# Kernel tuning notes

Measured on AMD Instinct MI355X. Metric: run time of the kernel, lower is better.

The kernel has to match this reference:

```python
import jax, jax.numpy as jnp
import numpy as np

DIL = 2      # dilation of deformable depthwise conv (padding == dilation -> same size)
EPS = 1e-5   # BatchNorm eps
B, C, O, G, H, W = 4, 256, 256, 64, 64, 64


def conv2d(x, w, padding, dilation=1):
    return jax.lax.conv_general_dilated(
        x, w, window_strides=(1, 1), padding=[(padding, padding)] * 2,
        rhs_dilation=(dilation, dilation),
        dimension_numbers=("NCHW", "OIHW", "NCHW"))


def bn_inf(x, gamma, beta, mean, var):
    scale = (gamma / jnp.sqrt(var + EPS))[None, :, None, None]
    return (x - mean[None, :, None, None]) * scale + beta[None, :, None, None]


def bilinear_gather(xt, ys, xs):
    # xt: [B,H,W,C]; ys, xs: [B,K,H,W] float sample coords. Zero padding outside.
    Bb, Hh, Ww, Cc = xt.shape
    y0 = jnp.floor(ys)
    x0 = jnp.floor(xs)
    wy = (ys - y0)[..., None]
    wx = (xs - x0)[..., None]
    bidx = jnp.arange(Bb)[:, None, None, None]

    def gather(yi, xi):
        valid = (yi >= 0) & (yi < Hh) & (xi >= 0) & (xi < Ww)
        yc = jnp.clip(yi, 0, Hh - 1).astype(jnp.int32)
        xc = jnp.clip(xi, 0, Ww - 1).astype(jnp.int32)
        val = xt[bidx, yc, xc]            # [B,K,H,W,C]
        return val * valid[..., None].astype(xt.dtype)

    v00 = gather(y0, x0)
    v01 = gather(y0, x0 + 1)
    v10 = gather(y0 + 1, x0)
    v11 = gather(y0 + 1, x0 + 1)
    return (v00 * (1 - wy) * (1 - wx) + v01 * (1 - wy) * wx
            + v10 * wy * (1 - wx) + v11 * wy * wx)


def setup_inputs() -> dict:
    key = jax.random.key(0)
    ks = jax.random.split(key, 12)
    inp = {
        "x": jax.random.normal(ks[0], (B, C, H, W), jnp.float32),
        "grad_feats": jax.random.normal(ks[1], (B, G, H, W), jnp.float32),
        # offset block: conv3x3(G->18) + BN + ReLU
        "off_w": jax.random.normal(ks[2], (18, G, 3, 3), jnp.float32) / np.sqrt(G * 9),
        "off_gamma": 1.0 + 0.1 * jax.random.normal(ks[3], (18,), jnp.float32),
        "off_beta": 0.1 * jax.random.normal(ks[4], (18,), jnp.float32),
        "off_mean": 0.1 * jax.random.normal(ks[5], (18,), jnp.float32),
        "off_var": jax.random.uniform(ks[6], (18,), jnp.float32, 0.5, 1.5),
        # deformable separable conv: depthwise 3x3 (per-channel) then pointwise 1x1, no bias
        "dw_w": jax.random.normal(ks[7], (C, 3, 3), jnp.float32) / 3.0,
        "pw_w": jax.random.normal(ks[8], (O, C), jnp.float32) / np.sqrt(C),
        # output BN
        "bn_gamma": 1.0 + 0.1 * jax.random.normal(ks[9], (O,), jnp.float32),
        "bn_beta": 0.1 * jax.random.normal(ks[10], (O,), jnp.float32),
        "bn_mean": 0.1 * jax.random.normal(ks[11], (O,), jnp.float32),
        "bn_var": jnp.ones((O,), jnp.float32),
    }
    return inp


def reference(x, grad_feats, off_w, off_gamma, off_beta, off_mean, off_var,
              dw_w, pw_w, bn_gamma, bn_beta, bn_mean, bn_var):
    Bb, Cc, Hh, Ww = x.shape
    # offset block: conv3x3 + BN + ReLU -> [B,18,H,W]
    off = jax.nn.relu(bn_inf(conv2d(grad_feats, off_w, 1),
                             off_gamma, off_beta, off_mean, off_var))
    off = off.reshape(Bb, 9, 2, Hh, Ww)
    dy, dx = off[:, :, 0], off[:, :, 1]                     # [B,9,H,W]
    # base kernel grid: padding == dilation so tap offsets are (kh-1)*DIL
    kk = (jnp.arange(3, dtype=jnp.float32) - 1.0) * DIL
    ky = jnp.repeat(kk, 3)                                   # [9] row offsets
    kx = jnp.tile(kk, 3)                                     # [9] col offsets
    gy = jnp.arange(Hh, dtype=jnp.float32)[None, None, :, None] + ky[None, :, None, None] + dy
    gx = jnp.arange(Ww, dtype=jnp.float32)[None, None, None, :] + kx[None, :, None, None] + dx
    samp = bilinear_gather(x.transpose(0, 2, 3, 1), gy, gx)  # [B,9,H,W,C]
    out = jnp.einsum("bkhwc,ck->bchw", samp, dw_w.reshape(Cc, 9))   # depthwise
    out = jnp.einsum("bchw,oc->bohw", out, pw_w)                    # pointwise 1x1
    out = jax.nn.relu(bn_inf(out, bn_gamma, bn_beta, bn_mean, bn_var))
    return out
```

## Files before the change

kernel.cpp:

```cpp
#include <hip/hip_runtime.h>
#include <stdint.h>

#define Bn 4
#define Cn 256
#define On 256
#define Gn 64
#define Hn 64
#define Wn 64
#define HWn 4096
#define EPSf 1e-5f

#define WS_XT    0u
#define WS_OFF   8388608u
#define WS_PWB   9568256u
#define WS_WT    9699328u

typedef __attribute__((ext_vector_type(8))) short short8;
typedef __attribute__((ext_vector_type(4))) float f4;

__device__ __forceinline__ unsigned int bfround(float f) {
    unsigned int u = __float_as_uint(f);
    u += 0x7FFFu + ((u >> 16) & 1u);
    return u >> 16;
}
__device__ __forceinline__ float blo(unsigned u) { return __uint_as_float(u << 16); }
__device__ __forceinline__ float bhi(unsigned u) { return __uint_as_float(u & 0xFFFF0000u); }

__global__ __launch_bounds__(256, 4) void k_pre(const float* __restrict__ x,
                                                const float* __restrict__ pw_w,
                                                const float* __restrict__ off_w,
                                                char* __restrict__ ws)
{
    __shared__ float smem[4160];
    int tid = threadIdx.x, bid = blockIdx.x;

    if (bid < 1024) {
        unsigned short* xt = (unsigned short*)(ws + WS_XT);
        int pt = bid & 63, ct = (bid >> 6) & 3, b = bid >> 8;
        int p0 = pt * 64, c0 = ct * 64;
        const f4* x4 = (const f4*)(x + (size_t)b * Cn * HWn);
        #pragma unroll
        for (int it = 0; it < 4; ++it) {
            int v = it * 256 + tid;
            int ci = v >> 4, pj = v & 15;
            f4 f = __builtin_nontemporal_load(&x4[(size_t)(c0 + ci) * 1024 + (p0 >> 2) + pj]);
            smem[ci * 65 + pj * 4 + 0] = f[0];
            smem[ci * 65 + pj * 4 + 1] = f[1];
            smem[ci * 65 + pj * 4 + 2] = f[2];
            smem[ci * 65 + pj * 4 + 3] = f[3];
        }
        __syncthreads();
        unsigned short* xtb = xt + (size_t)b * HWn * Cn;
        #pragma unroll
        for (int it = 0; it < 2; ++it) {
            int u = it * 256 + tid;
            int pi = u >> 3, cj = u & 7;
            float f[8];
            #pragma unroll
            for (int j = 0; j < 8; ++j)
                f[j] = smem[(cj * 8 + j) * 65 + pi];
            uint4 pk;
            pk.x = bfround(f[0]) | (bfround(f[1]) << 16);
            pk.y = bfround(f[2]) | (bfround(f[3]) << 16);
            pk.z = bfround(f[4]) | (bfround(f[5]) << 16);
            pk.w = bfround(f[6]) | (bfround(f[7]) << 16);
            *(uint4*)(xtb + (size_t)(p0 + pi) * Cn + c0 + cj * 8) = pk;
        }
        return;
    }
    if (bid < 1056) {
        unsigned short* pwb = (unsigned short*)(ws + WS_PWB);
        const float4* p4 = (const float4*)pw_w;
        uint2* o2 = (uint2*)pwb;
        int base = (bid - 1024) * 512;
        #pragma unroll
        for (int i = 0; i < 2; ++i) {
            int id2 = base + i * 256 + tid;
            float4 f = p4[id2];
            uint2 pk;
            pk.x = bfround(f.x) | (bfround(f.y) << 16);
            pk.y = bfround(f.z) | (bfround(f.w) << 16);
            o2[id2] = pk;
        }
        return;
    }
    {
        float* wT = (float*)(ws + WS_WT);
        for (int i = tid; i < 10368; i += 256) {
            int ch = i / 576;
            int rem = i - ch * 576;
            int g = rem / 9;
            int r9 = rem - g * 9;
            int ty = r9 / 3, tx = r9 - ty * 3;
            wT[(g * 3 + ty) * 54 + tx * 18 + ch] = off_w[i];
        }
    }
}

__global__ __launch_bounds__(256, 4) void k_off(const float* __restrict__ gf,
                                                const float* __restrict__ og,
                                                const float* __restrict__ obt,
                                                const float* __restrict__ om,
                                                const float* __restrict__ ov,
                                                char* __restrict__ ws)
{
    __shared__ float swt[10368];
    __shared__ float sred[4 * 18 * 65];
    const float* __restrict__ wT = (const float*)(ws + WS_WT);
    float* __restrict__ off = (float*)(ws + WS_OFF);
    int tid = threadIdx.x;
    int h = blockIdx.x, b = blockIdx.y;
    int lane = tid & 63;
    int wvU = __builtin_amdgcn_readfirstlane(tid >> 6);

    {
        const float4* w4 = (const float4*)wT;
        float4* s4 = (float4*)swt;
        #pragma unroll
        for (int j = 0; j < 11; ++j) {
            int idx = j * 256 + tid;
            if (idx < 2592) s4[idx] = w4[idx];
        }
    }
    __syncthreads();

    float acc[18];
    #pragma unroll
    for (int ch = 0; ch < 18; ++ch) acc[ch] = 0.f;

    const float* gfb = gf + (size_t)b * Gn * HWn;
    #pragma unroll 2
    for (int gi = 0; gi < 16; ++gi) {
        int g = wvU * 16 + gi;
        const float* gfg = gfb + (size_t)g * HWn;
        float rv[3], su[3], sd[3];
        #pragma unroll
        for (int r = 0; r < 3; ++r) {
            int y = h - 1 + r;
            rv[r] = ((unsigned)y < 64u) ? gfg[y * 64 + lane] : 0.f;
        }
        #pragma unroll
        for (int r = 0; r < 3; ++r) {
            float u = __shfl_up(rv[r], 1);   su[r] = (lane == 0)  ? 0.f : u;
            float d = __shfl_down(rv[r], 1); sd[r] = (lane == 63) ? 0.f : d;
        }
        #pragma unroll
        for (int ty = 0; ty < 3; ++ty) {
            const float* wrow = &swt[(g * 3 + ty) * 54];
            #pragma unroll
            for (int ch = 0; ch < 18; ++ch)
                acc[ch] += wrow[ch] * su[ty] + wrow[18 + ch] * rv[ty] + wrow[36 + ch] * sd[ty];
        }
    }

    #pragma unroll
    for (int ch = 0; ch < 18; ++ch)
        sred[(wvU * 18 + ch) * 65 + lane] = acc[ch];
    __syncthreads();

    float* obp = off + (size_t)(b * HWn + h * 64) * 18;
    for (int i = tid; i < 1152; i += 256) {
        int w = i / 18, ch = i - w * 18;
        float v = sred[ch * 65 + w] + sred[(18 + ch) * 65 + w]
                + sred[(36 + ch) * 65 + w] + sred[(54 + ch) * 65 + w];
        float s = og[ch] * rsqrtf(ov[ch] + EPSf);
        v = (v - om[ch]) * s + obt[ch];
        obp[i] = v > 0.f ? v : 0.f;
    }
}

#define TLD 264
__global__ __launch_bounds__(512, 4) void k_fuse(float* __restrict__ out,
                                                 const float* __restrict__ dw_w,
                                                 const float* __restrict__ bg,
                                                 const float* __restrict__ bb,
                                                 const float* __restrict__ bm,
                                                 const float* __restrict__ bv,
                                                 const char* __restrict__ ws)
{
    const unsigned short* __restrict__ xt  = (const unsigned short*)(ws + WS_XT);
    const unsigned short* __restrict__ pwb = (const unsigned short*)(ws + WS_PWB);
    const float* __restrict__ off = (const float*)(ws + WS_OFF);
    __shared__ float smeta[288 * 8];
    __shared__ float sdw[9 * 256];
    __shared__ unsigned short tl[32 * TLD];

    int bid = blockIdx.x;
    int xcd = bid & 7, slot = bid >> 3;
    int b = xcd >> 1;
    int h = ((xcd & 1) << 5) | (slot >> 1);
    int w0 = (slot & 1) << 5;
    int tid = threadIdx.x;

    for (int i = tid; i < 2304; i += 512) {
        int k = i >> 8, c = i & 255;
        sdw[i] = dw_w[c * 9 + k];
    }

    if (tid < 288) {
        int k = tid >> 5, wl = tid & 31;
        int w = w0 + wl;
        int kyi = k / 3, kxi = k - kyi * 3;
        const float* op = off + ((size_t)(b * HWn + h * 64 + w)) * 18 + 2 * k;
        float dy = op[0], dx = op[1];
        float gy = (float)(h + (kyi - 1) * 2) + dy;
        float gx = (float)(w + (kxi - 1) * 2) + dx;
        float fy = floorf(gy), fx = floorf(gx);
        float wy = gy - fy, wx = gx - fx;
        int y0 = (int)fy, x0 = (int)fx;
        int y1 = y0 + 1, x1 = x0 + 1;
        float m00 = ((unsigned)y0 < 64u && (unsigned)x0 < 64u) ? 1.f : 0.f;
        float m01 = ((unsigned)y0 < 64u && (unsigned)x1 < 64u) ? 1.f : 0.f;
        float m10 = ((unsigned)y1 < 64u && (unsigned)x0 < 64u) ? 1.f : 0.f;
        float m11 = ((unsigned)y1 < 64u && (unsigned)x1 < 64u) ? 1.f : 0.f;
        int y0c = min(max(y0, 0), 63), y1c = min(max(y1, 0), 63);
        int x0c = min(max(x0, 0), 63), x1c = min(max(x1, 0), 63);
        float4 mw;
        mw.x = (1.f - wy) * (1.f - wx) * m00;
        mw.y = (1.f - wy) * wx * m01;
        mw.z = wy * (1.f - wx) * m10;
        mw.w = wy * wx * m11;
        float4 mo;
        mo.x = __int_as_float((y0c * 64 + x0c) << 9);
        mo.y = __int_as_float((y0c * 64 + x1c) << 9);
        mo.z = __int_as_float((y1c * 64 + x0c) << 9);
        mo.w = __int_as_float((y1c * 64 + x1c) << 9);
        float4* s4w = (float4*)smeta;
        s4w[(k * 32 + wl) * 2] = mw;
        s4w[(k * 32 + wl) * 2 + 1] = mo;
    }
    __syncthreads();

    int lane = tid & 63, wave = tid >> 6;
    int half = lane >> 5, c8 = lane & 31;
    int c0 = c8 * 8;

    const char* xb = (const char*)(xt + (size_t)b * HWn * Cn);
    int laneByte = c8 * 16;
    const float4* s4 = (const float4*)smeta;
    #pragma unroll
    for (int iter = 0; iter < 2; ++iter) {
        int wl = iter * 16 + wave * 2 + half;
        float acc[8];
        #pragma unroll
        for (int j = 0; j < 8; ++j) acc[j] = 0.f;
        #pragma unroll 1
        for (int k = 0; k < 9; ++k) {
            float4 mw = s4[(k * 32 + wl) * 2];
            float4 mo = s4[(k * 32 + wl) * 2 + 1];
            float4 d0 = *(const float4*)(&sdw[k * 256 + c0]);
            float4 d1 = *(const float4*)(&sdw[k * 256 + c0 + 4]);
            uint4 qA = *(const uint4*)(xb + __float_as_int(mo.x) + laneByte);
            uint4 qB = *(const uint4*)(xb + __float_as_int(mo.y) + laneByte);
            uint4 qC = *(const uint4*)(xb + __float_as_int(mo.z) + laneByte);
            uint4 qD = *(const uint4*)(xb + __float_as_int(mo.w) + laneByte);
            const unsigned* uA = (const unsigned*)&qA;
            const unsigned* uB = (const unsigned*)&qB;
            const unsigned* uC = (const unsigned*)&qC;
            const unsigned* uD = (const unsigned*)&qD;
            const float* dk0 = (const float*)&d0;
            const float* dk1 = (const float*)&d1;
            #pragma unroll
            for (int j = 0; j < 4; ++j) {
                const float* dkj = (j < 2) ? dk0 : dk1;
                int jj = (j & 1) * 2;
                float sl = mw.x * blo(uA[j]) + mw.y * blo(uB[j]) + mw.z * blo(uC[j]) + mw.w * blo(uD[j]);
                float sh = mw.x * bhi(uA[j]) + mw.y * bhi(uB[j]) + mw.z * bhi(uC[j]) + mw.w * bhi(uD[j]);
                acc[2 * j]     += sl * dkj[jj];
                acc[2 * j + 1] += sh * dkj[jj + 1];
            }
        }
        uint4 pk;
        pk.x = bfround(acc[0]) | (bfround(acc[1]) << 16);
        pk.y = bfround(acc[2]) | (bfround(acc[3]) << 16);
        pk.z = bfround(acc[4]) | (bfround(acc[5]) << 16);
        pk.w = bfround(acc[6]) | (bfround(acc[7]) << 16);
        *(uint4*)(&tl[wl * TLD + c0]) = pk;
    }
    __syncthreads();

    int m0 = wave * 32;
    int row = lane & 15, quad = lane >> 4;
    f4 acc[2][2];
    #pragma unroll
    for (int i = 0; i < 2; ++i)
        #pragma unroll
        for (int j = 0; j < 2; ++j)
            acc[i][j] = (f4){0.f, 0.f, 0.f, 0.f};

    #pragma unroll 2
    for (int kq = 0; kq < 8; ++kq) {
        int kk = kq * 32 + quad * 8;
        short8 a[2], bf[2];
        #pragma unroll
        for (int mt = 0; mt < 2; ++mt)
            a[mt] = *(const short8*)(pwb + (size_t)(m0 + mt * 16 + row) * Cn + kk);
        #pragma unroll
        for (int nt = 0; nt < 2; ++nt)
            bf[nt] = *(const short8*)(&tl[(nt * 16 + row) * TLD + kk]);
        #pragma unroll
        for (int mt = 0; mt < 2; ++mt)
            #pragma unroll
            for (int nt = 0; nt < 2; ++nt)
                acc[mt][nt] = __builtin_amdgcn_mfma_f32_16x16x32_bf16(a[mt], bf[nt], acc[mt][nt], 0, 0, 0);
    }

    float* obp = out + (size_t)b * On * HWn + h * 64 + w0;
    #pragma unroll
    for (int mt = 0; mt < 2; ++mt) {
        #pragma unroll
        for (int r = 0; r < 4; ++r) {
            int o = m0 + mt * 16 + quad * 4 + r;
            float s = bg[o] * rsqrtf(bv[o] + EPSf);
            float sh = bb[o] - bm[o] * s;
            #pragma unroll
            for (int nt = 0; nt < 2; ++nt) {
                float v = acc[mt][nt][r] * s + sh;
                v = v > 0.f ? v : 0.f;
                __builtin_nontemporal_store(v, &obp[(size_t)o * HWn + nt * 16 + row]);
            }
        }
    }
}

extern "C" void kernel_launch(void* const* d_in, const int* in_sizes, int n_in,
                              void* d_out, int out_size, void* d_ws, size_t ws_size,
                              hipStream_t stream)
{
    const float* x     = (const float*)d_in[0];
    const float* gf    = (const float*)d_in[1];
    const float* off_w = (const float*)d_in[2];
    const float* og    = (const float*)d_in[3];
    const float* ob    = (const float*)d_in[4];
    const float* om    = (const float*)d_in[5];
    const float* ov    = (const float*)d_in[6];
    const float* dw_w  = (const float*)d_in[7];
    const float* pw_w  = (const float*)d_in[8];
    const float* bg    = (const float*)d_in[9];
    const float* bb    = (const float*)d_in[10];
    const float* bm    = (const float*)d_in[11];
    const float* bv    = (const float*)d_in[12];
    float* out = (float*)d_out;
    char* ws = (char*)d_ws;

    hipLaunchKernelGGL(k_pre, dim3(1057), dim3(256), 0, stream, x, pw_w, off_w, ws);
    hipLaunchKernelGGL(k_off, dim3(Hn, Bn), dim3(256), 0, stream,
                       gf, og, ob, om, ov, ws);
    hipLaunchKernelGGL(k_fuse, dim3(512), dim3(512), 0, stream,
                       out, dw_w, bg, bb, bm, bv, ws);
}
```

Baseline: 143.2 us.

## Read offset weights from global memory, raise fuse occupancy, simplify block mapping

k_off no longer stages the 41KB transposed offset-conv weights into LDS and reads them straight from global memory, relying on wave-uniform scalar loads. This drops the per-block copy and barrier and frees LDS for more resident blocks. k_fuse's launch bound rises from 4 to 6 blocks per CU, which may force register spills. Its XCD-aware block-to-tile mapping is replaced by a plain linear one, giving up L2 locality across XCDs.

New measurement: 153.0 us. +6.9%, slower.

```diff
diff --git a/kernel.cpp b/kernel.cpp
--- a/kernel.cpp
+++ b/kernel.cpp
@@ -98,38 +98,24 @@
 }
 
 __global__ __launch_bounds__(256, 4) void k_off(const float* __restrict__ gf,
+                                                const float* __restrict__ wT,
                                                 const float* __restrict__ og,
                                                 const float* __restrict__ obt,
                                                 const float* __restrict__ om,
                                                 const float* __restrict__ ov,
-                                                char* __restrict__ ws)
+                                                float* __restrict__ off)
 {
-    __shared__ float swt[10368];
     __shared__ float sred[4 * 18 * 65];
-    const float* __restrict__ wT = (const float*)(ws + WS_WT);
-    float* __restrict__ off = (float*)(ws + WS_OFF);
     int tid = threadIdx.x;
     int h = blockIdx.x, b = blockIdx.y;
     int lane = tid & 63;
     int wvU = __builtin_amdgcn_readfirstlane(tid >> 6);
 
-    {
-        const float4* w4 = (const float4*)wT;
-        float4* s4 = (float4*)swt;
-        #pragma unroll
-        for (int j = 0; j < 11; ++j) {
-            int idx = j * 256 + tid;
-            if (idx < 2592) s4[idx] = w4[idx];
-        }
-    }
-    __syncthreads();
-
     float acc[18];
     #pragma unroll
     for (int ch = 0; ch < 18; ++ch) acc[ch] = 0.f;
 
     const float* gfb = gf + (size_t)b * Gn * HWn;
-    #pragma unroll 2
     for (int gi = 0; gi < 16; ++gi) {
         int g = wvU * 16 + gi;
         const float* gfg = gfb + (size_t)g * HWn;
@@ -146,7 +132,7 @@
         }
         #pragma unroll
         for (int ty = 0; ty < 3; ++ty) {
-            const float* wrow = &swt[(g * 3 + ty) * 54];
+            const float* wrow = wT + (g * 3 + ty) * 54;
             #pragma unroll
             for (int ch = 0; ch < 18; ++ch)
                 acc[ch] += wrow[ch] * su[ty] + wrow[18 + ch] * rv[ty] + wrow[36 + ch] * sd[ty];
@@ -170,7 +156,7 @@
 }
 
 #define TLD 264
-__global__ __launch_bounds__(512, 4) void k_fuse(float* __restrict__ out,
+__global__ __launch_bounds__(512, 6) void k_fuse(float* __restrict__ out,
                                                  const float* __restrict__ dw_w,
                                                  const float* __restrict__ bg,
                                                  const float* __restrict__ bb,
@@ -186,10 +172,10 @@
     __shared__ unsigned short tl[32 * TLD];
 
     int bid = blockIdx.x;
-    int xcd = bid & 7, slot = bid >> 3;
-    int b = xcd >> 1;
-    int h = ((xcd & 1) << 5) | (slot >> 1);
-    int w0 = (slot & 1) << 5;
+    int b = bid >> 7;
+    int local = bid & 127;
+    int h = local >> 1;
+    int w0 = (local & 1) << 5;
     int tid = threadIdx.x;
 
     for (int i = tid; i < 2304; i += 512) {
@@ -345,7 +331,8 @@
 
     hipLaunchKernelGGL(k_pre, dim3(1057), dim3(256), 0, stream, x, pw_w, off_w, ws);
     hipLaunchKernelGGL(k_off, dim3(Hn, Bn), dim3(256), 0, stream,
-                       gf, og, ob, om, ov, ws);
+                       gf, (const float*)(ws + WS_WT), og, ob, om, ov,
+                       (float*)(ws + WS_OFF));
     hipLaunchKernelGGL(k_fuse, dim3(512), dim3(512), 0, stream,
                        out, dw_w, bg, bb, bm, bv, ws);
 }
```
